# Kernel optimization log

Measured on AMD Instinct MI355X. Metric: run time of the kernel, lower is better.

The kernel has to match this reference:

```python
import jax, jax.numpy as jnp
import numpy as np


def _kernel_mean(x, y, beta):
    # mean of exp(-beta * ||x_i - y_j||^2) over all pairs, without cdist call:
    x2 = jnp.sum(x * x, axis=1)  # [B1]
    y2 = jnp.sum(y * y, axis=1)  # [B2]
    d2 = x2[:, None] + y2[None, :] - 2.0 * jnp.einsum('id,jd->ij', x, y)
    d2 = jnp.maximum(d2, 0.0)
    return jnp.mean(jnp.exp(-beta * d2))


def setup_inputs() -> dict:
    key = jax.random.key(0)
    k1, k2 = jax.random.split(key)
    source = jax.random.normal(k1, (8192, 256), dtype=jnp.float32)
    target = jax.random.normal(k2, (8192, 256), dtype=jnp.float32)
    return {"source": source, "target": target}


def reference(source, target):
    sigma = 1.0
    beta = 1.0 / (2.0 * sigma)
    if source.ndim > 2:
        source = source.reshape(source.shape[0], -1)
    if target.ndim > 2:
        target = target.reshape(target.shape[0], -1)
    k_ss = _kernel_mean(source, source, beta)
    k_tt = _kernel_mean(target, target, beta)
    k_st = _kernel_mean(source, target, beta)
    return k_ss + k_tt - 2.0 * k_st
```

## Files before the change

kernel.cpp:

```cpp
#include <hip/hip_runtime.h>

#define NROWS 8192
#define DIM 256
#define NT 64
#define TRI ((NT * (NT + 1)) / 2)
#define NBLK (2 * TRI + NT * NT)

typedef __attribute__((ext_vector_type(4))) float f32x4;

#define NEGHALF_LOG2E (-0.72134752044448170368f)
#define LOG2E          (1.44269504088896340736f)

__global__ __launch_bounds__(256) void prep_kernel(
    const float* __restrict__ S, const float* __restrict__ T,
    unsigned* __restrict__ Sb, unsigned* __restrict__ Tb,
    float* __restrict__ x2s, float* __restrict__ x2t,
    float* __restrict__ accums) {
  if (blockIdx.x == 0 && threadIdx.x == 0) accums[0] = 0.f;
  const int w = threadIdx.x >> 6, l = threadIdx.x & 63;
  const int r = blockIdx.x * 4 + w;
  const float* src;
  unsigned* dst;
  float* sq;
  int row;
  if (r < NROWS) { src = S; dst = Sb; sq = x2s; row = r; }
  else           { src = T; dst = Tb; sq = x2t; row = r - NROWS; }

  const float4 v = *(const float4*)(src + (size_t)row * DIM + l * 4);
  int packed = __builtin_amdgcn_cvt_pk_fp8_f32(v.x, v.y, 0, false);
  packed = __builtin_amdgcn_cvt_pk_fp8_f32(v.z, v.w, packed, true);
  const float d0 = __builtin_amdgcn_cvt_f32_fp8(packed, 0);
  const float d1 = __builtin_amdgcn_cvt_f32_fp8(packed, 1);
  const float d2 = __builtin_amdgcn_cvt_f32_fp8(packed, 2);
  const float d3 = __builtin_amdgcn_cvt_f32_fp8(packed, 3);
  float s = d0 * d0 + d1 * d1 + d2 * d2 + d3 * d3;
  dst[(size_t)row * (DIM / 4) + l] = (unsigned)packed;
#pragma unroll
  for (int off = 32; off > 0; off >>= 1) s += __shfl_xor(s, off);
  if (l == 0) sq[row] = s * NEGHALF_LOG2E;
}

__device__ __forceinline__ void gload_lds16(const void* g, void* lds) {
  __builtin_amdgcn_global_load_lds(
      (const __attribute__((address_space(1))) unsigned int*)g,
      (__attribute__((address_space(3))) unsigned int*)lds, 16, 0, 0);
}

__global__ __launch_bounds__(256, 4) void mmd_gemm(
    const unsigned char* __restrict__ Sb, const unsigned char* __restrict__ Tb,
    const float* __restrict__ x2s, const float* __restrict__ x2t,
    float* __restrict__ accums) {
  __shared__ __align__(16) unsigned char lA[2][128 * 32];
  __shared__ __align__(16) unsigned char lB[2][128 * 32];
  __shared__ float lAx2[128];
  __shared__ float lBx2[128];
  __shared__ float wsum[4];

  const int tid = threadIdx.x;
  const int l = tid & 63;
  const int w = tid >> 6;
  const int wr = w >> 1, wc = w & 1;

  const int bid = blockIdx.x;
  const unsigned char* Ap;
  const unsigned char* Bp;
  const float* a2;
  const float* b2;
  int tr, tc;
  float wgt;
  if (bid < 2 * TRI) {
    const int i = (bid < TRI) ? bid : bid - TRI;
    int g = (int)((sqrtf((float)(8 * i + 1)) - 1.0f) * 0.5f);
    g = min(max(g - 2, 0), NT - 1);
    tr = g;
    while (tr < NT - 1 && (tr + 1) * (tr + 2) / 2 <= i) ++tr;
    tc = i - tr * (tr + 1) / 2;
    wgt = (tr == tc) ? 1.f : 2.f;
    if (bid < TRI) { Ap = Sb; Bp = Sb; a2 = x2s; b2 = x2s; }
    else           { Ap = Tb; Bp = Tb; a2 = x2t; b2 = x2t; }
  } else {
    const int t = bid - 2 * TRI;
    tr = t >> 6; tc = t & 63;
    wgt = -2.f;
    Ap = Sb; Bp = Tb; a2 = x2s; b2 = x2t;
  }

  const unsigned char* gA = Ap + (size_t)(tr * 128) * DIM;
  const unsigned char* gB = Bp + (size_t)(tc * 128) * DIM;

#define STAGE(buf, kt)                                                     \
  {                                                                        \
    const int row_ = tid >> 1, o_ = tid & 1;                               \
    const size_t go_ = (size_t)row_ * DIM + (kt) * 32 + o_ * 16;           \
    gload_lds16(gA + go_, &lA[buf][tid * 16]);                             \
    gload_lds16(gB + go_, &lB[buf][tid * 16]);                             \
  }

  STAGE(0, 0);

  if (tid < 128) lAx2[tid] = a2[tr * 128 + tid];
  else           lBx2[tid - 128] = b2[tc * 128 + tid - 128];

  f32x4 acc[4][4];
  const f32x4 zero = {0.f, 0.f, 0.f, 0.f};
#pragma unroll
  for (int m = 0; m < 4; ++m)
#pragma unroll
    for (int n = 0; n < 4; ++n) acc[m][n] = zero;

#pragma unroll
  for (int kt = 0; kt < 8; ++kt) {
    const int cur = kt & 1;
    asm volatile("s_waitcnt vmcnt(0)" ::: "memory");
    __builtin_amdgcn_s_barrier();
    asm volatile("" ::: "memory");
    if (kt < 7) STAGE(cur ^ 1, kt + 1);

    long af[4], bfv[4];
#pragma unroll
    for (int m = 0; m < 4; ++m) {
      const int row = wr * 64 + m * 16 + (l & 15);
      af[m] = *(const long*)&lA[cur][row * 32 + (l >> 4) * 8];
    }
#pragma unroll
    for (int n = 0; n < 4; ++n) {
      const int row = wc * 64 + n * 16 + (l & 15);
      bfv[n] = *(const long*)&lB[cur][row * 32 + (l >> 4) * 8];
    }
    __builtin_amdgcn_s_setprio(1);
#pragma unroll
    for (int m = 0; m < 4; ++m)
#pragma unroll
      for (int n = 0; n < 4; ++n)
        acc[m][n] = __builtin_amdgcn_mfma_f32_16x16x32_fp8_fp8(af[m], bfv[n], acc[m][n], 0, 0, 0);
    __builtin_amdgcn_s_setprio(0);
    asm volatile("" ::: "memory");
    __builtin_amdgcn_s_barrier();
  }

  float cb[4];
#pragma unroll
  for (int n = 0; n < 4; ++n) cb[n] = lBx2[wc * 64 + n * 16 + (l & 15)];
  float local = 0.f;
#pragma unroll
  for (int m = 0; m < 4; ++m) {
#pragma unroll
    for (int j = 0; j < 4; ++j) {
      const float rc = lAx2[wr * 64 + m * 16 + ((l >> 4) * 4 + j)];
#pragma unroll
      for (int n = 0; n < 4; ++n) {
        float arg = fmaf(LOG2E, acc[m][n][j], rc + cb[n]);
        arg = fminf(arg, 0.f);
        local += exp2f(arg);
      }
    }
  }
#pragma unroll
  for (int off = 32; off > 0; off >>= 1) local += __shfl_xor(local, off);
  if (l == 0) wsum[w] = local;
  __syncthreads();
  if (tid == 0) {
    atomicAdd(&accums[0], (wsum[0] + wsum[1] + wsum[2] + wsum[3]) * wgt);
  }
}

__global__ void finalize_kernel(const float* __restrict__ accums, float* __restrict__ out) {
  out[0] = accums[0] * (1.f / ((float)NROWS * (float)NROWS));
}

extern "C" void kernel_launch(void* const* d_in, const int* in_sizes, int n_in,
                              void* d_out, int out_size, void* d_ws, size_t ws_size,
                              hipStream_t stream) {
  const float* S = (const float*)d_in[0];
  const float* T = (const float*)d_in[1];
  float* out = (float*)d_out;

  unsigned char* Sb = (unsigned char*)d_ws;
  unsigned char* Tb = Sb + (size_t)NROWS * DIM;
  float* x2s = (float*)(Tb + (size_t)NROWS * DIM);
  float* x2t = x2s + NROWS;
  float* accums = x2t + NROWS;

  prep_kernel<<<(2 * NROWS) / 4, 256, 0, stream>>>(S, T, (unsigned*)Sb, (unsigned*)Tb,
                                                   x2s, x2t, accums);
  mmd_gemm<<<NBLK, 256, 0, stream>>>(Sb, Tb, x2s, x2t, accums);
  finalize_kernel<<<1, 1, 0, stream>>>(accums, out);
}
```

Baseline: 190.6 us.

## Pre-swizzle FP8 operands into MFMA fragment layout and load directly to registers

The prep kernel now writes FP8 rows in a panel layout grouped by 16-row blocks, arranged so each lane's MFMA A/B fragments for two k-steps sit in one contiguous 16-byte chunk. The GEMM kernel drops its LDS staging, barriers and async global-to-LDS loads, and instead double-buffers 16-byte global loads straight into registers. The row-norm terms are also read from global memory instead of LDS. This removes LDS traffic and block-wide synchronisation, but each wave now fetches its own operands from global memory with no sharing across waves, uses more registers (occupancy hint lowered from 4 to 3), and the prep kernel gains an LDS transpose pass.

```diff
diff --git a/kernel.cpp b/kernel.cpp
--- a/kernel.cpp
+++ b/kernel.cpp
@@ -7,53 +7,58 @@
 #define NBLK (2 * TRI + NT * NT)
 
 typedef __attribute__((ext_vector_type(4))) float f32x4;
+typedef __attribute__((ext_vector_type(2))) long long2v;
 
 #define NEGHALF_LOG2E (-0.72134752044448170368f)
 #define LOG2E          (1.44269504088896340736f)
 
 __global__ __launch_bounds__(256) void prep_kernel(
     const float* __restrict__ S, const float* __restrict__ T,
-    unsigned* __restrict__ Sb, unsigned* __restrict__ Tb,
+    unsigned char* __restrict__ Sb, unsigned char* __restrict__ Tb,
     float* __restrict__ x2s, float* __restrict__ x2t,
     float* __restrict__ accums) {
+  __shared__ unsigned char lds8[4][16][264];
   if (blockIdx.x == 0 && threadIdx.x == 0) accums[0] = 0.f;
   const int w = threadIdx.x >> 6, l = threadIdx.x & 63;
-  const int r = blockIdx.x * 4 + w;
+  const int pg = blockIdx.x * 4 + w;
   const float* src;
-  unsigned* dst;
+  unsigned char* dst;
   float* sq;
-  int row;
-  if (r < NROWS) { src = S; dst = Sb; sq = x2s; row = r; }
-  else           { src = T; dst = Tb; sq = x2t; row = r - NROWS; }
+  int p;
+  if (pg < 512) { src = S; dst = Sb; sq = x2s; p = pg; }
+  else          { src = T; dst = Tb; sq = x2t; p = pg - 512; }
+  const int r0 = p * 16;
 
-  const float4 v = *(const float4*)(src + (size_t)row * DIM + l * 4);
-  int packed = __builtin_amdgcn_cvt_pk_fp8_f32(v.x, v.y, 0, false);
-  packed = __builtin_amdgcn_cvt_pk_fp8_f32(v.z, v.w, packed, true);
-  const float d0 = __builtin_amdgcn_cvt_f32_fp8(packed, 0);
-  const float d1 = __builtin_amdgcn_cvt_f32_fp8(packed, 1);
-  const float d2 = __builtin_amdgcn_cvt_f32_fp8(packed, 2);
-  const float d3 = __builtin_amdgcn_cvt_f32_fp8(packed, 3);
-  float s = d0 * d0 + d1 * d1 + d2 * d2 + d3 * d3;
-  dst[(size_t)row * (DIM / 4) + l] = (unsigned)packed;
+  for (int r = 0; r < 16; ++r) {
+    const float4 v = *(const float4*)(src + (size_t)(r0 + r) * DIM + l * 4);
+    int pk = __builtin_amdgcn_cvt_pk_fp8_f32(v.x, v.y, 0, false);
+    pk = __builtin_amdgcn_cvt_pk_fp8_f32(v.z, v.w, pk, true);
+    *(unsigned*)&lds8[w][r][l * 4] = (unsigned)pk;
+    const float d0 = __builtin_amdgcn_cvt_f32_fp8(pk, 0);
+    const float d1 = __builtin_amdgcn_cvt_f32_fp8(pk, 1);
+    const float d2 = __builtin_amdgcn_cvt_f32_fp8(pk, 2);
+    const float d3 = __builtin_amdgcn_cvt_f32_fp8(pk, 3);
+    float s = d0 * d0 + d1 * d1 + d2 * d2 + d3 * d3;
 #pragma unroll
-  for (int off = 32; off > 0; off >>= 1) s += __shfl_xor(s, off);
-  if (l == 0) sq[row] = s * NEGHALF_LOG2E;
+    for (int off = 32; off > 0; off >>= 1) s += __shfl_xor(s, off);
+    if (l == 0) sq[r0 + r] = s * NEGHALF_LOG2E;
+  }
+  __syncthreads();
+
+  const int rr = l & 15, ss = l >> 4;
+#pragma unroll
+  for (int j = 0; j < 4; ++j) {
+    long2v o;
+    o[0] = *(const long*)&lds8[w][rr][(2 * j + 0) * 32 + ss * 8];
+    o[1] = *(const long*)&lds8[w][rr][(2 * j + 1) * 32 + ss * 8];
+    *(long2v*)(dst + (size_t)p * 4096 + j * 1024 + l * 16) = o;
+  }
 }
 
-__device__ __forceinline__ void gload_lds16(const void* g, void* lds) {
-  __builtin_amdgcn_global_load_lds(
-      (const __attribute__((address_space(1))) unsigned int*)g,
-      (__attribute__((address_space(3))) unsigned int*)lds, 16, 0, 0);
-}
-
-__global__ __launch_bounds__(256, 4) void mmd_gemm(
+__global__ __launch_bounds__(256, 3) void mmd_gemm(
     const unsigned char* __restrict__ Sb, const unsigned char* __restrict__ Tb,
     const float* __restrict__ x2s, const float* __restrict__ x2t,
     float* __restrict__ accums) {
-  __shared__ __align__(16) unsigned char lA[2][128 * 32];
-  __shared__ __align__(16) unsigned char lB[2][128 * 32];
-  __shared__ float lAx2[128];
-  __shared__ float lBx2[128];
   __shared__ float wsum[4];
 
   const int tid = threadIdx.x;
@@ -85,21 +90,8 @@
     Ap = Sb; Bp = Tb; a2 = x2s; b2 = x2t;
   }
 
-  const unsigned char* gA = Ap + (size_t)(tr * 128) * DIM;
-  const unsigned char* gB = Bp + (size_t)(tc * 128) * DIM;
-
-#define STAGE(buf, kt)                                                     \
-  {                                                                        \
-    const int row_ = tid >> 1, o_ = tid & 1;                               \
-    const size_t go_ = (size_t)row_ * DIM + (kt) * 32 + o_ * 16;           \
-    gload_lds16(gA + go_, &lA[buf][tid * 16]);                             \
-    gload_lds16(gB + go_, &lB[buf][tid * 16]);                             \
-  }
-
-  STAGE(0, 0);
-
-  if (tid < 128) lAx2[tid] = a2[tr * 128 + tid];
-  else           lBx2[tid - 128] = b2[tc * 128 + tid - 128];
+  const unsigned char* pA = Ap + ((size_t)(tr * 8 + wr * 4)) * 4096 + l * 16;
+  const unsigned char* pB = Bp + ((size_t)(tc * 8 + wc * 4)) * 4096 + l * 16;
 
   f32x4 acc[4][4];
   const f32x4 zero = {0.f, 0.f, 0.f, 0.f};
@@ -108,45 +100,41 @@
 #pragma unroll
     for (int n = 0; n < 4; ++n) acc[m][n] = zero;
 
+  long2v a4[2][4], b4[2][4];
+#define LOADP(buf, pr)                                                   \
+  {                                                                      \
+    _Pragma("unroll")                                                    \
+    for (int m = 0; m < 4; ++m) {                                        \
+      a4[buf][m] = *(const long2v*)(pA + m * 4096 + (pr) * 1024);        \
+      b4[buf][m] = *(const long2v*)(pB + m * 4096 + (pr) * 1024);        \
+    }                                                                    \
+  }
+
+  LOADP(0, 0);
 #pragma unroll
-  for (int kt = 0; kt < 8; ++kt) {
-    const int cur = kt & 1;
-    asm volatile("s_waitcnt vmcnt(0)" ::: "memory");
-    __builtin_amdgcn_s_barrier();
-    asm volatile("" ::: "memory");
-    if (kt < 7) STAGE(cur ^ 1, kt + 1);
-
-    long af[4], bfv[4];
+  for (int pr = 0; pr < 4; ++pr) {
+    const int cur = pr & 1;
+    if (pr < 3) LOADP(cur ^ 1, pr + 1);
 #pragma unroll
-    for (int m = 0; m < 4; ++m) {
-      const int row = wr * 64 + m * 16 + (l & 15);
-      af[m] = *(const long*)&lA[cur][row * 32 + (l >> 4) * 8];
-    }
+    for (int h = 0; h < 2; ++h)
 #pragma unroll
-    for (int n = 0; n < 4; ++n) {
-      const int row = wc * 64 + n * 16 + (l & 15);
-      bfv[n] = *(const long*)&lB[cur][row * 32 + (l >> 4) * 8];
-    }
-    __builtin_amdgcn_s_setprio(1);
+      for (int m = 0; m < 4; ++m)
 #pragma unroll
-    for (int m = 0; m < 4; ++m)
-#pragma unroll
-      for (int n = 0; n < 4; ++n)
-        acc[m][n] = __builtin_amdgcn_mfma_f32_16x16x32_fp8_fp8(af[m], bfv[n], acc[m][n], 0, 0, 0);
-    __builtin_amdgcn_s_setprio(0);
-    asm volatile("" ::: "memory");
-    __builtin_amdgcn_s_barrier();
+        for (int n = 0; n < 4; ++n)
+          acc[m][n] = __builtin_amdgcn_mfma_f32_16x16x32_fp8_fp8(
+              a4[cur][m][h], b4[cur][n][h], acc[m][n], 0, 0, 0);
   }
 
   float cb[4];
 #pragma unroll
-  for (int n = 0; n < 4; ++n) cb[n] = lBx2[wc * 64 + n * 16 + (l & 15)];
+  for (int n = 0; n < 4; ++n)
+    cb[n] = b2[tc * 128 + wc * 64 + n * 16 + (l & 15)];
   float local = 0.f;
 #pragma unroll
   for (int m = 0; m < 4; ++m) {
 #pragma unroll
     for (int j = 0; j < 4; ++j) {
-      const float rc = lAx2[wr * 64 + m * 16 + ((l >> 4) * 4 + j)];
+      const float rc = a2[tr * 128 + wr * 64 + m * 16 + (l >> 4) * 4 + j];
 #pragma unroll
       for (int n = 0; n < 4; ++n) {
         float arg = fmaf(LOG2E, acc[m][n][j], rc + cb[n]);
@@ -181,8 +169,7 @@
   float* x2t = x2s + NROWS;
   float* accums = x2t + NROWS;
 
-  prep_kernel<<<(2 * NROWS) / 4, 256, 0, stream>>>(S, T, (unsigned*)Sb, (unsigned*)Tb,
-                                                   x2s, x2t, accums);
+  prep_kernel<<<(2 * NROWS / 16) / 4, 256, 0, stream>>>(S, T, Sb, Tb, x2s, x2t, accums);
   mmd_gemm<<<NBLK, 256, 0, stream>>>(Sb, Tb, x2s, x2t, accums);
   finalize_kernel<<<1, 1, 0, stream>>>(accums, out);
 }
```

Result: faster. 184.4 us (-3.3%).
